# Performance work log

Hardware: AMD Instinct MI355X
Metric: run time of the kernel (lower is better)

The kernel has to match this reference:

```python
import jax, jax.numpy as jnp
import numpy as np

L, B, E, H, V, T = 512, 64, 256, 256, 32000, 50


def setup_inputs() -> dict:
    key = jax.random.key(0)
    ks = jax.random.split(key, 8)
    s_cell = 1.0 / np.sqrt(H + E)
    s_out = 1.0 / np.sqrt(2 * H)
    return {
        "text": jax.random.randint(ks[0], (L, B), 0, V, dtype=jnp.int64),
        "emb": jax.random.normal(ks[1], (V, E), dtype=jnp.float32),
        "W_f": jax.random.uniform(ks[2], (H, H + E), jnp.float32, -s_cell, s_cell),
        "b_f": jax.random.uniform(ks[3], (H,), jnp.float32, -s_cell, s_cell),
        "W_b": jax.random.uniform(ks[4], (H, H + E), jnp.float32, -s_cell, s_cell),
        "b_b": jax.random.uniform(ks[5], (H,), jnp.float32, -s_cell, s_cell),
        "W_out": jax.random.uniform(ks[6], (T, 2 * H), jnp.float32, -s_out, s_out),
        "b_out": jax.random.uniform(ks[7], (T,), jnp.float32, -s_out, s_out),
    }


def _rnn_scan(x_seq, W, b, batch, hidden):
    # x_seq: [L, B, E]; cell: h' = sigmoid(Linear(cat([x, h])))
    h0 = jnp.zeros((batch, hidden), dtype=x_seq.dtype)

    def step(h, x):
        h_new = jax.nn.sigmoid(jnp.concatenate([x, h], axis=1) @ W.T + b)
        return h_new, h_new

    _, hs = jax.lax.scan(step, h0, x_seq)
    return hs  # [L, B, H]


def reference(text, emb, W_f, b_f, W_b, b_b, W_out, b_out):
    # text: [L, B] int
    x = emb[text]  # [L, B, E]
    lr = _rnn_scan(x, W_f, b_f, x.shape[1], W_f.shape[0])  # [L, B, H]
    # backward cell processes reversed input; rl_tensor[i] = hidden after
    # processing positions L-1 .. L-1-i (NOT re-flipped, matching the source).
    rl = _rnn_scan(x[::-1], W_b, b_b, x.shape[1], W_b.shape[0])  # [L, B, H]
    hidden = jnp.concatenate([lr, rl], axis=2)  # [L, B, 2H]
    out = hidden @ W_out.T + b_out  # [L, B, T]
    return out, hidden
```

## Files before the change

### kernel.cpp

```cpp
#include <hip/hip_runtime.h>
#include <stdint.h>

#define L_SEQ 512
#define BATCH 64
#define KTOT  512
#define TDIM  50
#define HID2  512
#define ROWSTRIDE ((long)BATCH * HID2)

typedef __attribute__((ext_vector_type(8))) short bf16x8;
typedef __attribute__((ext_vector_type(4))) float f32x4;

static __device__ __forceinline__ unsigned short f2bf(float f) {
  union { float f; unsigned int u; } v; v.f = f;
  unsigned int r = (v.u + 0x7FFFu + ((v.u >> 16) & 1u)) >> 16;
  return (unsigned short)r;
}

static __device__ __forceinline__ bf16x8 pack8(const float* f) {
  bf16x8 r;
#pragma unroll
  for (int i = 0; i < 8; ++i) r[i] = (short)f2bf(f[i]);
  return r;
}

static __device__ __forceinline__ unsigned cvt_pk_bf16(float a, float b) {
  unsigned r;
  asm("v_cvt_pk_bf16_f32 %0, %1, %2" : "=v"(r) : "v"(a), "v"(b));
  return r;
}


__global__ __launch_bounds__(512) void pre_kernel(
    const int* __restrict__ text, const float* __restrict__ emb,
    const float* __restrict__ W_f, const float* __restrict__ b_f,
    const float* __restrict__ W_b, const float* __restrict__ b_b,
    float* __restrict__ hidden) {
  const int blk = blockIdx.x;
  const int dir = blk >> 8;
  const int base = (blk & 255) * 128;
  const float* W    = dir ? W_b : W_f;
  const float* bias = dir ? b_b : b_f;
  const int tid = threadIdx.x;
  const int w = tid >> 6, ln = tid & 63, m16 = ln & 15, g4 = ln >> 4;

  __shared__ __align__(16) unsigned char xLds[16 * 512];

  bf16x8 wfrag[2][8];
#pragma unroll
  for (int t = 0; t < 2; ++t) {
    const int j0 = w * 32 + t * 16 + m16;
#pragma unroll
    for (int kk = 0; kk < 8; ++kk) {
      const float* p = W + (long)j0 * KTOT + kk * 32 + g4 * 8;
      float4 p0 = *(const float4*)(p);
      float4 p1 = *(const float4*)(p + 4);
      float f[8] = {p0.x, p0.y, p0.z, p0.w, p1.x, p1.y, p1.z, p1.w};
      wfrag[t][kk] = pack8(f);
    }
  }
  float biasr[2][4];
#pragma unroll
  for (int t = 0; t < 2; ++t)
#pragma unroll
    for (int r = 0; r < 4; ++r) biasr[t][r] = bias[w * 32 + t * 16 + 4 * g4 + r];

  const int xm = tid >> 5;
  const int e0 = (tid & 31) * 8;

  for (int mt = 0; mt < 8; ++mt) {
    const int g = base + mt * 16 + xm;
    const int l = g >> 6, b = g & 63;
    const int srcl = dir ? (L_SEQ - 1 - l) : l;
    const int tok = text[srcl * BATCH + b];
    const float* xp = emb + (long)tok * 256 + e0;
    float4 a0 = *(const float4*)(xp);
    float4 a1 = *(const float4*)(xp + 4);
    float f[8] = {a0.x, a0.y, a0.z, a0.w, a1.x, a1.y, a1.z, a1.w};
    bf16x8 xv = pack8(f);
    if (mt) __syncthreads();
    *(bf16x8*)(xLds + xm * 512 + ((e0 * 2) ^ ((xm & 7) << 4))) = xv;
    __syncthreads();

    f32x4 acc0 = {0.f, 0.f, 0.f, 0.f};
    f32x4 acc1 = {0.f, 0.f, 0.f, 0.f};
#pragma unroll
    for (int kk = 0; kk < 8; ++kk) {
      bf16x8 uf = *(const bf16x8*)(xLds + m16 * 512 +
                                   (((kk * 64) + g4 * 16) ^ ((m16 & 7) << 4)));
      acc0 = __builtin_amdgcn_mfma_f32_16x16x32_bf16(wfrag[0][kk], uf, acc0, 0, 0, 0);
      acc1 = __builtin_amdgcn_mfma_f32_16x16x32_bf16(wfrag[1][kk], uf, acc1, 0, 0, 0);
    }
    const int gg = base + mt * 16 + m16;
    float* op = hidden + (long)gg * HID2 + dir * 256 + w * 32 + 4 * g4;
    *(float4*)(op)      = make_float4(acc0[0] + biasr[0][0], acc0[1] + biasr[0][1],
                                      acc0[2] + biasr[0][2], acc0[3] + biasr[0][3]);
    *(float4*)(op + 16) = make_float4(acc1[0] + biasr[1][0], acc1[1] + biasr[1][1],
                                      acc1[2] + biasr[1][2], acc1[3] + biasr[1][3]);
  }
}

__global__ __launch_bounds__(512, 1) void scan_kernel(
    const float* __restrict__ W_f, const float* __restrict__ W_b,
    float* __restrict__ hidden) {
  const int wg  = blockIdx.x;
  const int dir = wg >> 2;
  const int b0  = (wg & 3) * 16;
  const int tid = threadIdx.x;
  const int w = tid >> 6, ln = tid & 63, m16 = ln & 15, g4 = ln >> 4;
  const float* W = dir ? W_b : W_f;

  __shared__ __align__(16) unsigned char hLds[2][16 * 512];

  bf16x8 wfrag[2][8];
#pragma unroll
  for (int t = 0; t < 2; ++t) {
    const int j0 = w * 32 + t * 16 + m16;
#pragma unroll
    for (int kk = 0; kk < 8; ++kk) {
      const float* p = W + (long)j0 * KTOT + 256 + kk * 32 + g4 * 8;
      float4 p0 = *(const float4*)(p);
      float4 p1 = *(const float4*)(p + 4);
      float f[8] = {p0.x, p0.y, p0.z, p0.w, p1.x, p1.y, p1.z, p1.w};
      wfrag[t][kk] = pack8(f);
    }
  }

  const int swz = (m16 & 7) << 4;
  int rdoff[8];
#pragma unroll
  for (int kk = 0; kk < 8; ++kk)
    rdoff[kk] = m16 * 512 + ((kk * 64 + g4 * 16) ^ swz);
  const int wroff0 = m16 * 512 + ((w * 64 + g4 * 8) ^ swz);
  const int wroff1 = m16 * 512 + ((w * 64 + 32 + g4 * 8) ^ swz);

  *(f32x4*)(&hLds[0][0] + tid * 16) = f32x4{0.f, 0.f, 0.f, 0.f};

  const long roff = (long)(b0 + m16) * HID2 + dir * 256 + w * 32 + 4 * g4;

  f32x4 pA0, pA1, pB0, pB1;
  pA0 = *(const f32x4*)(hidden + roff);
  pA1 = *(const f32x4*)(hidden + roff + 16);
  pB0 = *(const f32x4*)(hidden + ROWSTRIDE + roff);
  pB1 = *(const f32x4*)(hidden + ROWSTRIDE + roff + 16);

  __syncthreads();

#define STEP(BUF, PF0, PF1, SROW)                                              \
  {                                                                            \
    bf16x8 uf[8];                                                              \
    _Pragma("unroll")                                                          \
    for (int kk = 0; kk < 8; ++kk)                                             \
      uf[kk] = *(const bf16x8*)(&hLds[BUF][0] + rdoff[kk]);                    \
    f32x4 acc0 = PF0, acc1 = PF1;                                              \
    _Pragma("unroll")                                                          \
    for (int kk = 0; kk < 8; ++kk) {                                           \
      acc0 = __builtin_amdgcn_mfma_f32_16x16x32_bf16(wfrag[0][kk], uf[kk],     \
                                                     acc0, 0, 0, 0);           \
      acc1 = __builtin_amdgcn_mfma_f32_16x16x32_bf16(wfrag[1][kk], uf[kk],     \
                                                     acc1, 0, 0, 0);           \
    }                                                                          \
    {                                                                          \
      const long rn = ((SROW) + 2 < L_SEQ) ? (SROW) + 2 : L_SEQ - 1;           \
      const float* lp = hidden + rn * ROWSTRIDE + roff;                        \
      PF0 = *(const f32x4*)(lp);                                               \
      PF1 = *(const f32x4*)(lp + 16);                                          \
    }                                                                          \
    float h0[4], h1[4];                                                        \
    _Pragma("unroll")                                                          \
    for (int r = 0; r < 4; ++r) {                                              \
      h0[r] = __builtin_amdgcn_rcpf(1.f + __expf(-acc0[r]));                   \
      h1[r] = __builtin_amdgcn_rcpf(1.f + __expf(-acc1[r]));                   \
    }                                                                          \
    *(uint2*)(&hLds[(BUF) ^ 1][0] + wroff0) =                                  \
        make_uint2(cvt_pk_bf16(h0[0], h0[1]), cvt_pk_bf16(h0[2], h0[3]));      \
    *(uint2*)(&hLds[(BUF) ^ 1][0] + wroff1) =                                  \
        make_uint2(cvt_pk_bf16(h1[0], h1[1]), cvt_pk_bf16(h1[2], h1[3]));      \
    float* gp = hidden + (long)(SROW)*ROWSTRIDE + roff;                        \
    *(float4*)(gp)      = make_float4(h0[0], h0[1], h0[2], h0[3]);             \
    *(float4*)(gp + 16) = make_float4(h1[0], h1[1], h1[2], h1[3]);             \
    asm volatile("s_waitcnt lgkmcnt(0)" ::: "memory");                         \
    __builtin_amdgcn_s_barrier();                                              \
    asm volatile("" ::: "memory");                                             \
  }

  for (int s = 0; s < L_SEQ; s += 2) {
    STEP(0, pA0, pA1, s)
    STEP(1, pB0, pB1, s + 1)
  }
#undef STEP
}

__global__ __launch_bounds__(64) void out_kernel(
    const float* __restrict__ hidden, const float* __restrict__ W_out,
    const float* __restrict__ b_out, float* __restrict__ out) {
  const int m0 = blockIdx.x * 16;
  const int ln = threadIdx.x;
  const int m16 = ln & 15, g4 = ln >> 4;

  bf16x8 a[16];
  const float* hp = hidden + (long)(m0 + m16) * HID2 + g4 * 8;
#pragma unroll
  for (int kk = 0; kk < 16; ++kk) {
    float4 p0 = *(const float4*)(hp + kk * 32);
    float4 p1 = *(const float4*)(hp + kk * 32 + 4);
    float f[8] = {p0.x, p0.y, p0.z, p0.w, p1.x, p1.y, p1.z, p1.w};
    a[kk] = pack8(f);
  }
#pragma unroll
  for (int nt = 0; nt < 4; ++nt) {
    const int trow = nt * 16 + m16;
    const bool valid = trow < TDIM;
    f32x4 acc = {0.f, 0.f, 0.f, 0.f};
    const float* wp = W_out + (long)trow * HID2 + g4 * 8;
#pragma unroll
    for (int kk = 0; kk < 16; ++kk) {
      bf16x8 bf;
      if (valid) {
        float4 p0 = *(const float4*)(wp + kk * 32);
        float4 p1 = *(const float4*)(wp + kk * 32 + 4);
        float f[8] = {p0.x, p0.y, p0.z, p0.w, p1.x, p1.y, p1.z, p1.w};
        bf = pack8(f);
      } else {
#pragma unroll
        for (int i = 0; i < 8; ++i) bf[i] = 0;
      }
      acc = __builtin_amdgcn_mfma_f32_16x16x32_bf16(a[kk], bf, acc, 0, 0, 0);
    }
    if (valid) {
      float bo = b_out[trow];
#pragma unroll
      for (int r = 0; r < 4; ++r)
        out[(long)(m0 + 4 * g4 + r) * TDIM + trow] = acc[r] + bo;
    }
  }
}

extern "C" void kernel_launch(void* const* d_in, const int* in_sizes, int n_in,
                              void* d_out, int out_size, void* d_ws, size_t ws_size,
                              hipStream_t stream) {
  const int*   text  = (const int*)d_in[0];
  const float* emb   = (const float*)d_in[1];
  const float* W_f   = (const float*)d_in[2];
  const float* b_f   = (const float*)d_in[3];
  const float* W_b   = (const float*)d_in[4];
  const float* b_b   = (const float*)d_in[5];
  const float* W_out = (const float*)d_in[6];
  const float* b_out = (const float*)d_in[7];
  float* out    = (float*)d_out;
  float* hidden = out + (long)L_SEQ * BATCH * TDIM;

  pre_kernel<<<512, 512, 0, stream>>>(text, emb, W_f, b_f, W_b, b_b, hidden);
  scan_kernel<<<8, 512, 0, stream>>>(W_f, W_b, hidden);
  out_kernel<<<2048, 64, 0, stream>>>(hidden, W_out, b_out, out);
}
```

Measured before the change: 481.9 us.

## Split scan steps across two wave groups and fold sigmoid scale into weights

The 8 waves of each scan workgroup are split into two groups of 4. Each group handles alternate timesteps and computes 64 hidden units per wave, so one group idles while the other works and its global prefetch of the next projected input is hidden across the idle phase. The -log2(e) factor is pre-multiplied into the recurrent weights and the precomputed input projections, so the sigmoid uses a raw exp2 with no per-element scaling. The cost is twice the weight fragments per wave (higher register pressure) and half the waves active per step.

```diff
diff --git a/kernel.cpp b/kernel.cpp
--- a/kernel.cpp
+++ b/kernel.cpp
@@ -7,6 +7,7 @@
 #define TDIM  50
 #define HID2  512
 #define ROWSTRIDE ((long)BATCH * HID2)
+#define NLOG2E 1.4426950408889634f
 
 typedef __attribute__((ext_vector_type(8))) short bf16x8;
 typedef __attribute__((ext_vector_type(4))) float f32x4;
@@ -93,14 +94,18 @@
     }
     const int gg = base + mt * 16 + m16;
     float* op = hidden + (long)gg * HID2 + dir * 256 + w * 32 + 4 * g4;
-    *(float4*)(op)      = make_float4(acc0[0] + biasr[0][0], acc0[1] + biasr[0][1],
-                                      acc0[2] + biasr[0][2], acc0[3] + biasr[0][3]);
-    *(float4*)(op + 16) = make_float4(acc1[0] + biasr[1][0], acc1[1] + biasr[1][1],
-                                      acc1[2] + biasr[1][2], acc1[3] + biasr[1][3]);
-  }
-}
-
-__global__ __launch_bounds__(512, 1) void scan_kernel(
+    *(float4*)(op)      = make_float4(-NLOG2E * (acc0[0] + biasr[0][0]),
+                                      -NLOG2E * (acc0[1] + biasr[0][1]),
+                                      -NLOG2E * (acc0[2] + biasr[0][2]),
+                                      -NLOG2E * (acc0[3] + biasr[0][3]));
+    *(float4*)(op + 16) = make_float4(-NLOG2E * (acc1[0] + biasr[1][0]),
+                                      -NLOG2E * (acc1[1] + biasr[1][1]),
+                                      -NLOG2E * (acc1[2] + biasr[1][2]),
+                                      -NLOG2E * (acc1[3] + biasr[1][3]));
+  }
+}
+
+__global__ __launch_bounds__(512, 2) void scan_kernel(
     const float* __restrict__ W_f, const float* __restrict__ W_b,
     float* __restrict__ hidden) {
   const int wg  = blockIdx.x;
@@ -108,20 +113,23 @@
   const int b0  = (wg & 3) * 16;
   const int tid = threadIdx.x;
   const int w = tid >> 6, ln = tid & 63, m16 = ln & 15, g4 = ln >> 4;
+  const int grp = w >> 2;
+  const int wq  = w & 3;
   const float* W = dir ? W_b : W_f;
 
   __shared__ __align__(16) unsigned char hLds[2][16 * 512];
 
-  bf16x8 wfrag[2][8];
-#pragma unroll
-  for (int t = 0; t < 2; ++t) {
-    const int j0 = w * 32 + t * 16 + m16;
+  bf16x8 wfrag[4][8];
+#pragma unroll
+  for (int t = 0; t < 4; ++t) {
+    const int j0 = wq * 64 + t * 16 + m16;
 #pragma unroll
     for (int kk = 0; kk < 8; ++kk) {
       const float* p = W + (long)j0 * KTOT + 256 + kk * 32 + g4 * 8;
       float4 p0 = *(const float4*)(p);
       float4 p1 = *(const float4*)(p + 4);
-      float f[8] = {p0.x, p0.y, p0.z, p0.w, p1.x, p1.y, p1.z, p1.w};
+      float f[8] = {-NLOG2E * p0.x, -NLOG2E * p0.y, -NLOG2E * p0.z, -NLOG2E * p0.w,
+                    -NLOG2E * p1.x, -NLOG2E * p1.y, -NLOG2E * p1.z, -NLOG2E * p1.w};
       wfrag[t][kk] = pack8(f);
     }
   }
@@ -131,62 +139,61 @@
 #pragma unroll
   for (int kk = 0; kk < 8; ++kk)
     rdoff[kk] = m16 * 512 + ((kk * 64 + g4 * 16) ^ swz);
-  const int wroff0 = m16 * 512 + ((w * 64 + g4 * 8) ^ swz);
-  const int wroff1 = m16 * 512 + ((w * 64 + 32 + g4 * 8) ^ swz);
+  int wroff[4];
+#pragma unroll
+  for (int t = 0; t < 4; ++t)
+    wroff[t] = m16 * 512 + ((wq * 128 + t * 32 + g4 * 8) ^ swz);
 
   *(f32x4*)(&hLds[0][0] + tid * 16) = f32x4{0.f, 0.f, 0.f, 0.f};
 
-  const long roff = (long)(b0 + m16) * HID2 + dir * 256 + w * 32 + 4 * g4;
-
-  f32x4 pA0, pA1, pB0, pB1;
-  pA0 = *(const f32x4*)(hidden + roff);
-  pA1 = *(const f32x4*)(hidden + roff + 16);
-  pB0 = *(const f32x4*)(hidden + ROWSTRIDE + roff);
-  pB1 = *(const f32x4*)(hidden + ROWSTRIDE + roff + 16);
+  const long roff = (long)(b0 + m16) * HID2 + dir * 256 + wq * 64 + 4 * g4;
+
+  f32x4 pf[4];
+#pragma unroll
+  for (int t = 0; t < 4; ++t)
+    pf[t] = *(const f32x4*)(hidden + (long)grp * ROWSTRIDE + roff + t * 16);
 
   __syncthreads();
 
-#define STEP(BUF, PF0, PF1, SROW)                                              \
+#define STEP(BUFR, BUFW, SROW)                                                 \
   {                                                                            \
     bf16x8 uf[8];                                                              \
     _Pragma("unroll")                                                          \
     for (int kk = 0; kk < 8; ++kk)                                             \
-      uf[kk] = *(const bf16x8*)(&hLds[BUF][0] + rdoff[kk]);                    \
-    f32x4 acc0 = PF0, acc1 = PF1;                                              \
+      uf[kk] = *(const bf16x8*)(&hLds[BUFR][0] + rdoff[kk]);                   \
     _Pragma("unroll")                                                          \
-    for (int kk = 0; kk < 8; ++kk) {                                           \
-      acc0 = __builtin_amdgcn_mfma_f32_16x16x32_bf16(wfrag[0][kk], uf[kk],     \
-                                                     acc0, 0, 0, 0);           \
-      acc1 = __builtin_amdgcn_mfma_f32_16x16x32_bf16(wfrag[1][kk], uf[kk],     \
-                                                     acc1, 0, 0, 0);           \
+    for (int t = 0; t < 4; ++t)                                                \
+      _Pragma("unroll")                                                        \
+      for (int kk = 0; kk < 8; ++kk)                                           \
+        pf[t] = __builtin_amdgcn_mfma_f32_16x16x32_bf16(wfrag[t][kk], uf[kk],  \
+                                                        pf[t], 0, 0, 0);       \
+    float* gp = hidden + (long)(SROW)*ROWSTRIDE + roff;                        \
+    _Pragma("unroll")                                                          \
+    for (int t = 0; t < 4; ++t) {                                              \
+      float h[4];                                                              \
+      _Pragma("unroll")                                                        \
+      for (int r = 0; r < 4; ++r)                                              \
+        h[r] = __builtin_amdgcn_rcpf(1.f + __builtin_amdgcn_exp2f(pf[t][r]));  \
+      *(uint2*)(&hLds[BUFW][0] + wroff[t]) =                                   \
+          make_uint2(cvt_pk_bf16(h[0], h[1]), cvt_pk_bf16(h[2], h[3]));        \
+      *(float4*)(gp + t * 16) = make_float4(h[0], h[1], h[2], h[3]);           \
     }                                                                          \
     {                                                                          \
       const long rn = ((SROW) + 2 < L_SEQ) ? (SROW) + 2 : L_SEQ - 1;           \
       const float* lp = hidden + rn * ROWSTRIDE + roff;                        \
-      PF0 = *(const f32x4*)(lp);                                               \
-      PF1 = *(const f32x4*)(lp + 16);                                          \
+      _Pragma("unroll")                                                        \
+      for (int t = 0; t < 4; ++t) pf[t] = *(const f32x4*)(lp + t * 16);        \
     }                                                                          \
-    float h0[4], h1[4];                                                        \
-    _Pragma("unroll")                                                          \
-    for (int r = 0; r < 4; ++r) {                                              \
-      h0[r] = __builtin_amdgcn_rcpf(1.f + __expf(-acc0[r]));                   \
-      h1[r] = __builtin_amdgcn_rcpf(1.f + __expf(-acc1[r]));                   \
-    }                                                                          \
-    *(uint2*)(&hLds[(BUF) ^ 1][0] + wroff0) =                                  \
-        make_uint2(cvt_pk_bf16(h0[0], h0[1]), cvt_pk_bf16(h0[2], h0[3]));      \
-    *(uint2*)(&hLds[(BUF) ^ 1][0] + wroff1) =                                  \
-        make_uint2(cvt_pk_bf16(h1[0], h1[1]), cvt_pk_bf16(h1[2], h1[3]));      \
-    float* gp = hidden + (long)(SROW)*ROWSTRIDE + roff;                        \
-    *(float4*)(gp)      = make_float4(h0[0], h0[1], h0[2], h0[3]);             \
-    *(float4*)(gp + 16) = make_float4(h1[0], h1[1], h1[2], h1[3]);             \
     asm volatile("s_waitcnt lgkmcnt(0)" ::: "memory");                         \
-    __builtin_amdgcn_s_barrier();                                              \
-    asm volatile("" ::: "memory");                                             \
   }
 
   for (int s = 0; s < L_SEQ; s += 2) {
-    STEP(0, pA0, pA1, s)
-    STEP(1, pB0, pB1, s + 1)
+    if (grp == 0) STEP(0, 1, s)
+    __builtin_amdgcn_s_barrier();
+    asm volatile("" ::: "memory");
+    if (grp == 1) STEP(1, 0, s + 1)
+    __builtin_amdgcn_s_barrier();
+    asm volatile("" ::: "memory");
   }
 #undef STEP
 }
```

Result: slower. 589.5 us (+22.3%).
